# Performance work log

Hardware: AMD Instinct MI355X
Metric: run time of the kernel (lower is better)

## Reference

```python
import jax, jax.numpy as jnp
import numpy as np

EMB, QK, V, H = 1024, 64, 64, 16
B, S = 4, 2048


def setup_inputs() -> dict:
    key = jax.random.key(0)
    ks = jax.random.split(key, 8)
    sc = 0.02
    x_q = jax.random.normal(ks[0], (B, S, EMB), jnp.float32)
    x_k_v = jax.random.normal(ks[1], (B, S, EMB), jnp.float32)
    # causal mask: True means masked (matches torch masked_fill)
    causal = ~jnp.tril(jnp.ones((S, S), dtype=bool))
    attn_mask = jnp.broadcast_to(causal, (B, S, S))
    w_q = jax.random.normal(ks[2], (H * QK, EMB), jnp.float32) * sc
    b_q = jnp.zeros((H * QK,), jnp.float32)
    w_k = jax.random.normal(ks[3], (H * QK, EMB), jnp.float32) * sc
    b_k = jnp.zeros((H * QK,), jnp.float32)
    w_v = jax.random.normal(ks[4], (H * V, EMB), jnp.float32) * sc
    b_v = jnp.zeros((H * V,), jnp.float32)
    return {"x_q": x_q, "x_k_v": x_k_v, "attn_mask": attn_mask,
            "w_q": w_q, "b_q": b_q, "w_k": w_k, "b_k": b_k, "w_v": w_v, "b_v": b_v}


def reference(x_q, x_k_v, attn_mask, w_q, b_q, w_k, b_k, w_v, b_v):
    Bq, Sq, _ = x_q.shape
    Skv = x_k_v.shape[1]
    q = (x_q @ w_q.T + b_q).reshape(Bq, Sq, H, QK).transpose(0, 2, 1, 3)   # [B,H,Sq,QK]
    k = (x_k_v @ w_k.T + b_k).reshape(Bq, Skv, H, QK).transpose(0, 2, 1, 3)  # [B,H,Skv,QK]
    v = (x_k_v @ w_v.T + b_v).reshape(Bq, Skv, H, V).transpose(0, 2, 1, 3)   # [B,H,Skv,V]
    attn = jnp.einsum('bhqd,bhkd->bhqk', q, k) / jnp.sqrt(jnp.float32(QK))
    attn = jnp.where(attn_mask[:, None, :, :], jnp.float32(-1e9), attn)
    attn = jax.nn.softmax(attn, axis=-1)
    z = jnp.einsum('bhqk,bhkv->bhqv', attn, v)        # [B,H,Sq,V]
    z = z.transpose(0, 2, 1, 3).reshape(Bq, Sq, H * V)
    return z
```

## Files before the change

kernel.cpp:

```cpp
#include <hip/hip_runtime.h>

#define B_    4
#define H_    16
#define S_    2048
#define EMB_  1024
#define D_    64

typedef __attribute__((ext_vector_type(4))) float f32x4;
typedef __attribute__((ext_vector_type(8))) short frag_ab;
typedef unsigned short ushort_t;

__device__ __forceinline__ unsigned short f2bf(float f) {
    unsigned int u = __float_as_uint(f);
    unsigned int r = u + 0x7fffu + ((u >> 16) & 1u);
    return (unsigned short)(r >> 16);
}
__device__ __forceinline__ unsigned short f2bf_fast(float f) {
    return (unsigned short)((__float_as_uint(f) + 0x8000u) >> 16);
}

__device__ __forceinline__ void gld16(const void* g, void* l) {
    __builtin_amdgcn_global_load_lds(
        (const __attribute__((address_space(1))) void*)g,
        (__attribute__((address_space(3))) void*)l, 16, 0, 0);
}

#define SCOL(lane) ((((lane) & 7) ^ (((lane) >> 3) & 7)) * 8)

#define QSCALE (0.125f * 1.44269504089f)

__global__ void cvt_all(const float* __restrict__ s0, const float* __restrict__ s1,
                        const float* __restrict__ s2, const float* __restrict__ s3,
                        const float* __restrict__ s4,
                        ushort_t* __restrict__ d0, ushort_t* __restrict__ d1,
                        ushort_t* __restrict__ d2, ushort_t* __restrict__ d3,
                        ushort_t* __restrict__ d4) {
    const int b = blockIdx.x;
    const float* src; ushort_t* dst; int i;
    float mul = 1.0f;
    if (b < 3072) {
        const int z = b >> 10;
        src = (z == 0) ? s0 : (z == 1 ? s1 : s2);
        dst = (z == 0) ? d0 : (z == 1 ? d1 : d2);
        if (z == 0) mul = QSCALE;
        i = (b & 1023) * 256 + threadIdx.x;
    } else {
        const int b2 = b - 3072;
        const int z = b2 >> 13;
        src = z ? s4 : s3;
        dst = z ? d4 : d3;
        i = (b2 & 8191) * 256 + threadIdx.x;
    }
    float4 f = ((const float4*)src)[i];
    ushort4 o;
    o.x = f2bf(f.x * mul); o.y = f2bf(f.y * mul);
    o.z = f2bf(f.z * mul); o.w = f2bf(f.w * mul);
    ((ushort4*)dst)[i] = o;
}

__global__ __launch_bounds__(256) void qkv_gemm(
    const ushort_t* __restrict__ xq,
    const ushort_t* __restrict__ xkv,
    const ushort_t* __restrict__ wq,
    const ushort_t* __restrict__ wk,
    const ushort_t* __restrict__ wv,
    const float* __restrict__ bq,
    const float* __restrict__ bk,
    const float* __restrict__ bv,
    ushort_t* __restrict__ qo,
    ushort_t* __restrict__ ko,
    ushort_t* __restrict__ vto)
{
    __shared__ ushort_t As[2][128 * 64];
    __shared__ ushort_t Bs[2][128 * 64];

    const int id = blockIdx.x;
    const int xcd = id & 7, j = id >> 3;
    const int m_t = xcd * 8 + (j & 7);
    const int n_t = (j >> 3) & 7;
    const int z   = j >> 6;

    const ushort_t* A = (z == 0) ? xq : xkv;
    const ushort_t* W = (z == 0) ? wq : (z == 1 ? wk : wv);
    const float* bias = (z == 0) ? bq : (z == 1 ? bk : bv);
    const float scale = (z == 0) ? QSCALE : 1.0f;

    const int tid = threadIdx.x;
    const int m0 = m_t * 128, n0 = n_t * 128;
    const int w = tid >> 6, lane = tid & 63, quad = lane >> 4, l16 = lane & 15;
    const int wm = w & 1, wn = w >> 1;
    const int scol = SCOL(lane);

    f32x4 acc[4][4];
#pragma unroll
    for (int i = 0; i < 4; ++i)
#pragma unroll
        for (int j2 = 0; j2 < 4; ++j2) acc[i][j2] = (f32x4){0.f, 0.f, 0.f, 0.f};

    const ushort_t* pa = A + (size_t)(m0 + w * 32 + (lane >> 3)) * EMB_ + scol;
    const ushort_t* pw = W + (size_t)(n0 + w * 32 + (lane >> 3)) * EMB_ + scol;

    auto stage = [&](int bsel, int kt) {
        const int k0 = kt * 64;
#pragma unroll
        for (int i = 0; i < 4; ++i) {
            const int base = w * 32 + i * 8;
            gld16(pa + (size_t)(i * 8) * EMB_ + k0, &As[bsel][base * 64]);
            gld16(pw + (size_t)(i * 8) * EMB_ + k0, &Bs[bsel][base * 64]);
        }
    };

    const int key = l16 & 7;
    stage(0, 0);
    for (int kt = 0; kt < 16; ++kt) {
        __syncthreads();
        if (kt < 15) stage((kt + 1) & 1, kt + 1);
        const int bsel = kt & 1;

#pragma unroll
        for (int c = 0; c < 2; ++c) {
            const int boff = ((c * 4 + quad) ^ key) * 8;
            frag_ab a[4], bfr[4];
#pragma unroll
            for (int t = 0; t < 4; ++t) {
                a[t]   = *(const frag_ab*)&As[bsel][(wm * 64 + t * 16 + l16) * 64 + boff];
                bfr[t] = *(const frag_ab*)&Bs[bsel][(wn * 64 + t * 16 + l16) * 64 + boff];
            }
#pragma unroll
            for (int tm = 0; tm < 4; ++tm)
#pragma unroll
                for (int tn = 0; tn < 4; ++tn)
                    acc[tm][tn] = __builtin_amdgcn_mfma_f32_16x16x32_bf16(
                        a[tm], bfr[tn], acc[tm][tn], 0, 0, 0);
        }
    }

    if (z == 2) {
#pragma unroll
        for (int tn = 0; tn < 4; ++tn) {
            int n = n0 + wn * 64 + tn * 16 + l16;
            float bval = bias[n];
            int hh = n >> 6, dd = n & 63;
#pragma unroll
            for (int tm = 0; tm < 4; ++tm) {
                int m = m0 + wm * 64 + tm * 16 + quad * 4;
                int bb = m >> 11, ss = m & (S_ - 1);
                union { ushort4 v; ushort_t u[4]; } pk;
#pragma unroll
                for (int r = 0; r < 4; ++r) pk.u[r] = f2bf(acc[tm][tn][r] + bval);
                *(ushort4*)&vto[(((size_t)bb * H_ + hh) * D_ + dd) * S_ + ss] = pk.v;
            }
        }
    } else {
        ushort_t* ob = (z == 0) ? qo : ko;
#pragma unroll
        for (int tn = 0; tn < 4; ++tn) {
            int n = n0 + wn * 64 + tn * 16 + l16;
            float bvalS = bias[n] * scale;
            int hh = n >> 6, dd = n & 63;
#pragma unroll
            for (int tm = 0; tm < 4; ++tm) {
#pragma unroll
                for (int r = 0; r < 4; ++r) {
                    int m = m0 + wm * 64 + tm * 16 + quad * 4 + r;
                    int bb = m >> 11, ss = m & (S_ - 1);
                    float val = acc[tm][tn][r] + bvalS;
                    ob[(((size_t)bb * H_ + hh) * S_ + ss) * D_ + dd] = f2bf(val);
                }
            }
        }
    }
}

__global__ __launch_bounds__(256) void attn_kernel(
    const ushort_t* __restrict__ qg,
    const ushort_t* __restrict__ kg,
    const ushort_t* __restrict__ vtg,
    float* __restrict__ out)
{
    __shared__ ushort_t Kt[2][64 * 64];
    __shared__ ushort_t Vt[2][64 * 64];
    __shared__ ushort_t Pb[4][32 * 64];

    const int tid = threadIdx.x;
    const int w = tid >> 6, lane = tid & 63, quad = lane >> 4, l16 = lane & 15;
    const int scol = SCOL(lane);

    const int id = blockIdx.x;
    const int rr = id >> 3;
    const int bh = (id & 7) + 8 * (rr & 7);
    const int qi = 15 - (rr >> 3);
    const int q0 = qi * 128;
    const int b = bh >> 4, h = bh & 15;

    const ushort_t* qp  = qg  + (size_t)bh * S_ * D_;
    const ushort_t* kp  = kg  + (size_t)bh * S_ * D_;
    const ushort_t* vtp = vtg + (size_t)bh * D_ * S_;

    frag_ab aq[2][2];
#pragma unroll
    for (int rg = 0; rg < 2; ++rg) {
        const ushort_t* qr = qp + (size_t)(q0 + rg * 64 + w * 16 + l16) * D_;
        aq[rg][0] = *(const frag_ab*)(qr + quad * 8);
        aq[rg][1] = *(const frag_ab*)(qr + 32 + quad * 8);
    }

    frag_ab ones;
#pragma unroll
    for (int i = 0; i < 8; ++i) ones[i] = (short)0x3F80;

    f32x4 o[2][4];
    f32x4 osum[2];
#pragma unroll
    for (int rg = 0; rg < 2; ++rg) {
        osum[rg] = (f32x4){0.f, 0.f, 0.f, 0.f};
#pragma unroll
        for (int t = 0; t < 4; ++t) o[rg][t] = (f32x4){0.f, 0.f, 0.f, 0.f};
    }

    ushort_t* Pw = &Pb[w][0];
    const int last = 2 * qi + 1;

    auto stage = [&](int bsel, int kt) {
#pragma unroll
        for (int i = 0; i < 2; ++i) {
            const int base = w * 16 + i * 8;
            gld16(kp  + (size_t)(kt * 64 + base + (lane >> 3)) * D_ + scol,
                  &Kt[bsel][base * 64]);
            gld16(vtp + (size_t)(base + (lane >> 3)) * S_ + kt * 64 + scol,
                  &Vt[bsel][base * 64]);
        }
    };

    const int key = l16 & 7;
    stage(0, 0);
    for (int kt = 0; kt <= last; ++kt) {
        __syncthreads();
        if (kt < last) stage((kt + 1) & 1, kt + 1);
        const int bsel = kt & 1;

        frag_ab bk[4][2], bv[4][2];
#pragma unroll
        for (int t = 0; t < 4; ++t) {
#pragma unroll
            for (int hf = 0; hf < 2; ++hf) {
                const int off = (t * 16 + l16) * 64 + ((hf * 4 + quad) ^ key) * 8;
                bk[t][hf] = *(const frag_ab*)&Kt[bsel][off];
                bv[t][hf] = *(const frag_ab*)&Vt[bsel][off];
            }
        }

#pragma unroll
        for (int rg = 0; rg < 2; ++rg) {
            if (rg == 0 && kt == last) continue;
            const bool diag = (kt == 2 * qi + rg);
            f32x4 scf[4];
            __builtin_amdgcn_s_setprio(1);
#pragma unroll
            for (int tn = 0; tn < 4; ++tn) {
                f32x4 sc = (f32x4){0.f, 0.f, 0.f, 0.f};
                sc = __builtin_amdgcn_mfma_f32_16x16x32_bf16(aq[rg][0], bk[tn][0], sc, 0, 0, 0);
                sc = __builtin_amdgcn_mfma_f32_16x16x32_bf16(aq[rg][1], bk[tn][1], sc, 0, 0, 0);
                scf[tn] = sc;
            }
            __builtin_amdgcn_s_setprio(0);
            if (diag) {
#pragma unroll
                for (int tn = 0; tn < 4; ++tn) {
                    int kcol = kt * 64 + tn * 16 + l16;
#pragma unroll
                    for (int r = 0; r < 4; ++r) {
                        int qrow = q0 + rg * 64 + w * 16 + quad * 4 + r;
                        if (kcol > qrow) scf[tn][r] = -1e30f;
                    }
                }
            }
#pragma unroll
            for (int r = 0; r < 4; ++r) {
                const int prow = rg * 16 + quad * 4 + r;
                const int rowoff = prow * 64 + (l16 & 7);
                const int pkey = prow & 7;
#pragma unroll
                for (int tn = 0; tn < 4; ++tn) {
                    float p = __builtin_amdgcn_exp2f(scf[tn][r]);
                    Pw[rowoff + ((tn * 2 + (l16 >> 3)) ^ pkey) * 8] = f2bf_fast(p);
                }
            }
        }
        asm volatile("s_waitcnt lgkmcnt(0)" ::: "memory");
#pragma unroll
        for (int rg = 0; rg < 2; ++rg) {
            if (rg == 0 && kt == last) continue;
            const int poff = (rg * 16 + l16) * 64;
            frag_ab ap0 = *(const frag_ab*)&Pw[poff + ((0 + quad) ^ key) * 8];
            frag_ab ap1 = *(const frag_ab*)&Pw[poff + ((4 + quad) ^ key) * 8];
            __builtin_amdgcn_s_setprio(1);
#pragma unroll
            for (int tv = 0; tv < 4; ++tv) {
                o[rg][tv] = __builtin_amdgcn_mfma_f32_16x16x32_bf16(ap0, bv[tv][0], o[rg][tv], 0, 0, 0);
                o[rg][tv] = __builtin_amdgcn_mfma_f32_16x16x32_bf16(ap1, bv[tv][1], o[rg][tv], 0, 0, 0);
            }
            osum[rg] = __builtin_amdgcn_mfma_f32_16x16x32_bf16(ap0, ones, osum[rg], 0, 0, 0);
            osum[rg] = __builtin_amdgcn_mfma_f32_16x16x32_bf16(ap1, ones, osum[rg], 0, 0, 0);
            __builtin_amdgcn_s_setprio(0);
        }
    }

    float* ob = out + (size_t)b * S_ * (H_ * D_) + h * D_;
#pragma unroll
    for (int rg = 0; rg < 2; ++rg) {
#pragma unroll
        for (int r = 0; r < 4; ++r) {
            float inv = 1.0f / osum[rg][r];
            int srow = q0 + rg * 64 + w * 16 + quad * 4 + r;
#pragma unroll
            for (int tv = 0; tv < 4; ++tv)
                ob[(size_t)srow * (H_ * D_) + tv * 16 + l16] = o[rg][tv][r] * inv;
        }
    }
}

extern "C" void kernel_launch(void* const* d_in, const int* in_sizes, int n_in,
                              void* d_out, int out_size, void* d_ws, size_t ws_size,
                              hipStream_t stream) {
    const float* x_q  = (const float*)d_in[0];
    const float* x_kv = (const float*)d_in[1];
    const float* w_q  = (const float*)d_in[3];
    const float* b_q  = (const float*)d_in[4];
    const float* w_k  = (const float*)d_in[5];
    const float* b_k  = (const float*)d_in[6];
    const float* w_v  = (const float*)d_in[7];
    const float* b_v  = (const float*)d_in[8];
    float* out = (float*)d_out;

    ushort_t* ws  = (ushort_t*)d_ws;
    ushort_t* wqb = ws;
    ushort_t* wkb = wqb + 1048576;
    ushort_t* wvb = wkb + 1048576;
    ushort_t* xqb  = wvb + 1048576;
    ushort_t* xkvb = xqb + 8388608;
    ushort_t* qb   = xkvb + 8388608;
    ushort_t* kb   = qb + 8388608;
    ushort_t* vtb  = kb + 8388608;

    cvt_all<<<19456, 256, 0, stream>>>(
        w_q, w_k, w_v, x_q, x_kv, wqb, wkb, wvb, xqb, xkvb);
    qkv_gemm<<<1536, 256, 0, stream>>>(
        xqb, xkvb, wqb, wkb, wvb, b_q, b_k, b_v, qb, kb, vtb);
    attn_kernel<<<1024, 256, 0, stream>>>(qb, kb, vtb, out);
}
```

Before: 290.7 us.

## Restructure QKV GEMM into 256x128 tiles with 8 waves and interleaved prefetch

```diff
diff --git a/kernel.cpp b/kernel.cpp
--- a/kernel.cpp
+++ b/kernel.cpp
@@ -58,7 +58,7 @@
     ((ushort4*)dst)[i] = o;
 }
 
-__global__ __launch_bounds__(256) void qkv_gemm(
+__global__ __launch_bounds__(512) void qkv_gemm(
     const ushort_t* __restrict__ xq,
     const ushort_t* __restrict__ xkv,
     const ushort_t* __restrict__ wq,
@@ -71,14 +71,15 @@
     ushort_t* __restrict__ ko,
     ushort_t* __restrict__ vto)
 {
-    __shared__ ushort_t As[2][128 * 64];
+    __shared__ ushort_t As[2][256 * 64];
     __shared__ ushort_t Bs[2][128 * 64];
 
     const int id = blockIdx.x;
-    const int xcd = id & 7, j = id >> 3;
-    const int m_t = xcd * 8 + (j & 7);
-    const int n_t = (j >> 3) & 7;
-    const int z   = j >> 6;
+    const int xcd = id & 7;
+    const int j = id >> 3;
+    const int m_t = xcd * 4 + (j & 3);
+    const int n_t = (j >> 2) & 7;
+    const int z   = j >> 5;
 
     const ushort_t* A = (z == 0) ? xq : xkv;
     const ushort_t* W = (z == 0) ? wq : (z == 1 ? wk : wv);
@@ -86,85 +87,112 @@
     const float scale = (z == 0) ? QSCALE : 1.0f;
 
     const int tid = threadIdx.x;
-    const int m0 = m_t * 128, n0 = n_t * 128;
     const int w = tid >> 6, lane = tid & 63, quad = lane >> 4, l16 = lane & 15;
     const int wm = w & 1, wn = w >> 1;
     const int scol = SCOL(lane);
-
-    f32x4 acc[4][4];
-#pragma unroll
-    for (int i = 0; i < 4; ++i)
-#pragma unroll
-        for (int j2 = 0; j2 < 4; ++j2) acc[i][j2] = (f32x4){0.f, 0.f, 0.f, 0.f};
+    const int m0 = m_t * 256, n0 = n_t * 128;
+    const int key = l16 & 7;
+
+    f32x4 acc[8][2];
+#pragma unroll
+    for (int i = 0; i < 8; ++i)
+#pragma unroll
+        for (int k = 0; k < 2; ++k) acc[i][k] = (f32x4){0.f, 0.f, 0.f, 0.f};
 
     const ushort_t* pa = A + (size_t)(m0 + w * 32 + (lane >> 3)) * EMB_ + scol;
-    const ushort_t* pw = W + (size_t)(n0 + w * 32 + (lane >> 3)) * EMB_ + scol;
-
-    auto stage = [&](int bsel, int kt) {
-        const int k0 = kt * 64;
-#pragma unroll
-        for (int i = 0; i < 4; ++i) {
-            const int base = w * 32 + i * 8;
-            gld16(pa + (size_t)(i * 8) * EMB_ + k0, &As[bsel][base * 64]);
-            gld16(pw + (size_t)(i * 8) * EMB_ + k0, &Bs[bsel][base * 64]);
-        }
-    };
-
-    const int key = l16 & 7;
-    stage(0, 0);
-    for (int kt = 0; kt < 16; ++kt) {
-        __syncthreads();
-        if (kt < 15) stage((kt + 1) & 1, kt + 1);
-        const int bsel = kt & 1;
-
-#pragma unroll
-        for (int c = 0; c < 2; ++c) {
-            const int boff = ((c * 4 + quad) ^ key) * 8;
-            frag_ab a[4], bfr[4];
-#pragma unroll
-            for (int t = 0; t < 4; ++t) {
-                a[t]   = *(const frag_ab*)&As[bsel][(wm * 64 + t * 16 + l16) * 64 + boff];
-                bfr[t] = *(const frag_ab*)&Bs[bsel][(wn * 64 + t * 16 + l16) * 64 + boff];
-            }
-#pragma unroll
-            for (int tm = 0; tm < 4; ++tm)
-#pragma unroll
-                for (int tn = 0; tn < 4; ++tn)
-                    acc[tm][tn] = __builtin_amdgcn_mfma_f32_16x16x32_bf16(
-                        a[tm], bfr[tn], acc[tm][tn], 0, 0, 0);
-        }
+    const ushort_t* pw = W + (size_t)(n0 + w * 16 + (lane >> 3)) * EMB_ + scol;
+
+    auto stageA = [&](int bsel, int kt, int i) {
+        gld16(pa + (size_t)(i * 8) * EMB_ + kt * 64, &As[bsel][(w * 32 + i * 8) * 64]);
+    };
+    auto stageB = [&](int bsel, int kt, int i) {
+        gld16(pw + (size_t)(i * 8) * EMB_ + kt * 64, &Bs[bsel][(w * 16 + i * 8) * 64]);
+    };
+    auto ldA = [&](int cur, int fm, int c) -> frag_ab {
+        return *(const frag_ab*)&As[cur][(wm * 128 + fm * 16 + l16) * 64 +
+                                         (((c * 4 + quad) ^ key) * 8)];
+    };
+
+    auto ktile = [&](const int cur, const int t) {
+        const int nxt = cur ^ 1;
+        const bool pf = (t < 15);
+        frag_ab bfr[2][2];
+#pragma unroll
+        for (int fn = 0; fn < 2; ++fn)
+#pragma unroll
+            for (int c = 0; c < 2; ++c)
+                bfr[fn][c] = *(const frag_ab*)&Bs[cur][(wn * 32 + fn * 16 + l16) * 64 +
+                                                       (((c * 4 + quad) ^ key) * 8)];
+#pragma unroll
+        for (int p = 0; p < 4; ++p) {
+            frag_ab a0c0 = ldA(cur, 2 * p,     0);
+            frag_ab a0c1 = ldA(cur, 2 * p,     1);
+            frag_ab a1c0 = ldA(cur, 2 * p + 1, 0);
+            frag_ab a1c1 = ldA(cur, 2 * p + 1, 1);
+            if (pf) {
+                if (p == 0)      { stageA(nxt, t + 1, 0); stageA(nxt, t + 1, 1); }
+                else if (p == 1) { stageA(nxt, t + 1, 2); stageA(nxt, t + 1, 3); }
+                else if (p == 2) { stageB(nxt, t + 1, 0); stageB(nxt, t + 1, 1); }
+            }
+            __builtin_amdgcn_s_barrier();
+            asm volatile("s_waitcnt lgkmcnt(0)" ::: "memory");
+            __builtin_amdgcn_sched_barrier(0);
+            __builtin_amdgcn_s_setprio(1);
+            acc[2*p  ][0] = __builtin_amdgcn_mfma_f32_16x16x32_bf16(a0c0, bfr[0][0], acc[2*p  ][0], 0, 0, 0);
+            acc[2*p  ][1] = __builtin_amdgcn_mfma_f32_16x16x32_bf16(a0c0, bfr[1][0], acc[2*p  ][1], 0, 0, 0);
+            acc[2*p+1][0] = __builtin_amdgcn_mfma_f32_16x16x32_bf16(a1c0, bfr[0][0], acc[2*p+1][0], 0, 0, 0);
+            acc[2*p+1][1] = __builtin_amdgcn_mfma_f32_16x16x32_bf16(a1c0, bfr[1][0], acc[2*p+1][1], 0, 0, 0);
+            acc[2*p  ][0] = __builtin_amdgcn_mfma_f32_16x16x32_bf16(a0c1, bfr[0][1], acc[2*p  ][0], 0, 0, 0);
+            acc[2*p  ][1] = __builtin_amdgcn_mfma_f32_16x16x32_bf16(a0c1, bfr[1][1], acc[2*p  ][1], 0, 0, 0);
+            acc[2*p+1][0] = __builtin_amdgcn_mfma_f32_16x16x32_bf16(a1c1, bfr[0][1], acc[2*p+1][0], 0, 0, 0);
+            acc[2*p+1][1] = __builtin_amdgcn_mfma_f32_16x16x32_bf16(a1c1, bfr[1][1], acc[2*p+1][1], 0, 0, 0);
+            __builtin_amdgcn_s_setprio(0);
+            if (p == 3 && pf) asm volatile("s_waitcnt vmcnt(0)" ::: "memory");
+            __builtin_amdgcn_s_barrier();
+        }
+    };
+
+#pragma unroll
+    for (int i = 0; i < 4; ++i) stageA(0, 0, i);
+    stageB(0, 0, 0); stageB(0, 0, 1);
+    asm volatile("s_waitcnt vmcnt(0)" ::: "memory");
+    __builtin_amdgcn_s_barrier();
+
+    for (int tt = 0; tt < 8; ++tt) {
+        ktile(0, 2 * tt);
+        ktile(1, 2 * tt + 1);
     }
 
     if (z == 2) {
 #pragma unroll
-        for (int tn = 0; tn < 4; ++tn) {
-            int n = n0 + wn * 64 + tn * 16 + l16;
+        for (int fn = 0; fn < 2; ++fn) {
+            int n = n0 + wn * 32 + fn * 16 + l16;
             float bval = bias[n];
             int hh = n >> 6, dd = n & 63;
 #pragma unroll
-            for (int tm = 0; tm < 4; ++tm) {
-                int m = m0 + wm * 64 + tm * 16 + quad * 4;
+            for (int fm = 0; fm < 8; ++fm) {
+                int m = m0 + wm * 128 + fm * 16 + quad * 4;
                 int bb = m >> 11, ss = m & (S_ - 1);
                 union { ushort4 v; ushort_t u[4]; } pk;
 #pragma unroll
-                for (int r = 0; r < 4; ++r) pk.u[r] = f2bf(acc[tm][tn][r] + bval);
+                for (int r = 0; r < 4; ++r) pk.u[r] = f2bf(acc[fm][fn][r] + bval);
                 *(ushort4*)&vto[(((size_t)bb * H_ + hh) * D_ + dd) * S_ + ss] = pk.v;
             }
         }
     } else {
         ushort_t* ob = (z == 0) ? qo : ko;
 #pragma unroll
-        for (int tn = 0; tn < 4; ++tn) {
-            int n = n0 + wn * 64 + tn * 16 + l16;
+        for (int fn = 0; fn < 2; ++fn) {
+            int n = n0 + wn * 32 + fn * 16 + l16;
             float bvalS = bias[n] * scale;
             int hh = n >> 6, dd = n & 63;
 #pragma unroll
-            for (int tm = 0; tm < 4; ++tm) {
+            for (int fm = 0; fm < 8; ++fm) {
 #pragma unroll
                 for (int r = 0; r < 4; ++r) {
-                    int m = m0 + wm * 64 + tm * 16 + quad * 4 + r;
+                    int m = m0 + wm * 128 + fm * 16 + quad * 4 + r;
                     int bb = m >> 11, ss = m & (S_ - 1);
-                    float val = acc[tm][tn][r] + bvalS;
+                    float val = acc[fm][fn][r] + bvalS;
                     ob[(((size_t)bb * H_ + hh) * S_ + ss) * D_ + dd] = f2bf(val);
                 }
             }
@@ -345,7 +373,7 @@
 
     cvt_all<<<19456, 256, 0, stream>>>(
         w_q, w_k, w_v, x_q, x_kv, wqb, wkb, wvb, xqb, xkvb);
-    qkv_gemm<<<1536, 256, 0, stream>>>(
+    qkv_gemm<<<768, 512, 0, stream>>>(
         xqb, xkvb, wqb, wkb, wvb, b_q, b_k, b_v, qb, kb, vtb);
     attn_kernel<<<1024, 256, 0, stream>>>(qb, kb, vtb, out);
 }
```

Measured after the change: 307.9 us. 5.9% more time.
